# Optimization experiments

Measured on AMD Instinct MI355X. Metric: run time of the kernel, lower is better.

Reference implementation:

```python
import jax, jax.numpy as jnp
import numpy as np

T, B, D, H = 256, 128, 128, 1024
MEL = 48           # preprocess.melodyRange
MELODY_COEFF = 0.5
FORGET_BIAS = 1.0  # TF BasicLSTMCell default


def setup_inputs() -> dict:
    key = jax.random.key(0)
    ks = jax.random.split(key, 8)
    s = 0.05
    return {
        "inSeq": jax.random.normal(ks[0], (T, B, D), dtype=jnp.float32),
        "targetSeq": jax.random.randint(ks[1], (T, B, 2), 0, MEL).astype(jnp.int64),
        "W1": jax.random.normal(ks[2], (D + H, 4 * H), dtype=jnp.float32) * s,
        "b1": jnp.zeros((4 * H,), dtype=jnp.float32),
        "W2": jax.random.normal(ks[3], (2 * H, 4 * H), dtype=jnp.float32) * s,
        "b2": jnp.zeros((4 * H,), dtype=jnp.float32),
        "outW": jax.random.normal(ks[4], (H, D), dtype=jnp.float32) * s,
        "outB": jnp.zeros((D,), dtype=jnp.float32),
    }


def _lstm_cell(x, c, h, W, b):
    # TF BasicLSTMCell: gates in (i, j, f, o) order, forget_bias added to f
    z = jnp.concatenate([x, h], axis=-1) @ W + b
    i, j, f, o = jnp.split(z, 4, axis=-1)
    c_new = c * jax.nn.sigmoid(f + FORGET_BIAS) + jax.nn.sigmoid(i) * jnp.tanh(j)
    h_new = jnp.tanh(c_new) * jax.nn.sigmoid(o)
    return c_new, h_new


def _forward(inSeq, targetSeq, W1, b1, W2, b2, outW, outB):
    dt = inSeq.dtype
    zero = jnp.zeros((B, H), dtype=dt)

    def step(carry, x):
        c1, h1, c2, h2 = carry
        c1, h1 = _lstm_cell(x, c1, h1, W1, b1)
        c2, h2 = _lstm_cell(h1, c2, h2, W2, b2)
        return (c1, h1, c2, h2), h2

    _, outputs = jax.lax.scan(step, (zero, zero, zero, zero), inSeq)  # [T,B,H]
    logits = outputs @ outW + outB                                    # [T,B,D]

    mel_logits = logits[..., :MEL]
    har_logits = logits[..., MEL:]

    # probs: per-timestep dual softmax, concatenated
    probs = jnp.concatenate(
        [jax.nn.softmax(mel_logits, axis=-1), jax.nn.softmax(har_logits, axis=-1)],
        axis=-1,
    )

    # dual sparse softmax cross-entropy
    mel_lp = jax.nn.log_softmax(mel_logits, axis=-1)
    har_lp = jax.nn.log_softmax(har_logits, axis=-1)
    mel_ce = -jnp.take_along_axis(mel_lp, targetSeq[..., 0:1], axis=-1)[..., 0]
    har_ce = -jnp.take_along_axis(har_lp, targetSeq[..., 1:2], axis=-1)[..., 0]
    losses = MELODY_COEFF * mel_ce + (1.0 - MELODY_COEFF) * har_ce
    loss = jnp.sum(losses) / T / B
    return probs, loss


def reference(inSeq, targetSeq, W1, b1, W2, b2, outW, outB):
    return _forward(inSeq, targetSeq, W1, b1, W2, b2, outW, outB)
```

## Files before the change

kernel.cpp:

```cpp
#include <hip/hip_runtime.h>
#include <cstdint>
#include <cstddef>

#define T_ 256
#define B_ 128
#define D_ 128
#define H_ 1024
#define K1_ 1152
#define K2_ 2048

#define R_ 32

typedef __bf16 bf16x8 __attribute__((ext_vector_type(8)));
typedef short s8 __attribute__((ext_vector_type(8)));
typedef float f32x4 __attribute__((ext_vector_type(4)));

__device__ __forceinline__ unsigned short f2bf(float f) {
  unsigned int u = __builtin_bit_cast(unsigned int, f);
  u += 0x7fff + ((u >> 16) & 1);
  return (unsigned short)(u >> 16);
}
__device__ __forceinline__ float sigm(float x) { return 1.f / (1.f + __expf(-x)); }
__device__ __forceinline__ float tanh_(float x) { return 1.f - 2.f / (__expf(2.f * x) + 1.f); }

__device__ __forceinline__ f32x4 mfma16(s8 a, s8 b, f32x4 c) {
  return __builtin_amdgcn_mfma_f32_16x16x32_bf16(
      __builtin_bit_cast(bf16x8, a), __builtin_bit_cast(bf16x8, b), c, 0, 0, 0);
}

__device__ __forceinline__ void st_bypass_short(unsigned short* p, unsigned int v) {
  asm volatile("global_store_short %0, %1, off sc0 sc1" :: "v"(p), "v"(v) : "memory");
}
__device__ __forceinline__ void st_flag(int* p, int v) {
  asm volatile("global_store_dword %0, %1, off sc0 sc1" :: "v"(p), "v"(v) : "memory");
}

__device__ __forceinline__ void wave_wait1(const int* p, int want) {
  for (;;) {
    int4 v;
    asm volatile("global_load_dwordx4 %0, %1, off sc0 sc1\n\ts_waitcnt vmcnt(0)"
                 : "=v"(v) : "v"(p) : "memory");
    int ok = (v.x >= want) && (v.y >= want) && (v.z >= want) && (v.w >= want);
    if (__all(ok)) break;
    __builtin_amdgcn_s_sleep(1);
  }
}
__device__ __forceinline__ void wave_wait2(const int* pa, int wa,
                                           const int* pb, int wb) {
  for (;;) {
    int4 a, b;
    asm volatile("global_load_dwordx4 %0, %2, off sc0 sc1\n\t"
                 "global_load_dwordx4 %1, %3, off sc0 sc1\n\t"
                 "s_waitcnt vmcnt(0)"
                 : "=v"(a), "=v"(b) : "v"(pa), "v"(pb) : "memory");
    int ok = (a.x >= wa) && (a.y >= wa) && (a.z >= wa) && (a.w >= wa) &&
             (b.x >= wb) && (b.y >= wb) && (b.z >= wb) && (b.w >= wb);
    if (__all(ok)) break;
    __builtin_amdgcn_s_sleep(1);
  }
}

__global__ void prep_misc(const float* __restrict__ inSeq,
                          const float* __restrict__ outW,
                          unsigned short* __restrict__ xbf,
                          unsigned short* __restrict__ outWp,
                          unsigned short* __restrict__ h1b,
                          unsigned short* __restrict__ h1r,
                          unsigned short* __restrict__ h2all,
                          float* __restrict__ c1, float* __restrict__ c2,
                          float* __restrict__ loss,
                          int* __restrict__ f1, int* __restrict__ f2)
{
  int i = blockIdx.x * 256 + threadIdx.x;
  if (i < T_ * B_ * D_) xbf[i] = f2bf(inSeq[i]);
  if (i < B_ * H_) {
    c1[i] = 0.f; c2[i] = 0.f;
    h1b[B_ * H_ + i] = 0;
    if (h1r) h1r[(size_t)(R_ - 1) * B_ * H_ + i] = 0;
    h2all[i] = 0;
  }
  if (i < H_ * D_) {
    int c = i >> 10, k = i & 1023;
    outWp[i] = f2bf(outW[(size_t)k * D_ + c]);
  }
  if (f1 && i < 256) { f1[i] = 0; f2[i] = 0; }
  if (i == 0) loss[0] = 0.f;
}

__global__ void pack_w(const float* __restrict__ src, unsigned short* __restrict__ dst, int K)
{
  __shared__ float tile[64][65];
  int k0 = blockIdx.x * 64, j0 = blockIdx.y * 64, g = blockIdx.z;
  int tid = threadIdx.x;
#pragma unroll
  for (int e = 0; e < 16; ++e) {
    int li = e * 256 + tid;
    int kl = li >> 6, jl = li & 63;
    tile[kl][jl] = src[(size_t)(k0 + kl) * 4096 + g * 1024 + j0 + jl];
  }
  __syncthreads();
#pragma unroll
  for (int e = 0; e < 16; ++e) {
    int li = e * 256 + tid;
    int jl = li >> 6, kl = li & 63;
    dst[(size_t)((j0 + jl) * 4 + g) * K + k0 + kl] = f2bf(tile[kl][jl]);
  }
}

__global__ __launch_bounds__(256, 2) void phase_kernel(
    int p,
    const unsigned short* __restrict__ xbf,
    const unsigned short* __restrict__ W1p,
    const unsigned short* __restrict__ W2p,
    const float* __restrict__ b1,
    const float* __restrict__ b2,
    unsigned short* __restrict__ h1b,
    unsigned short* __restrict__ h2all,
    float* __restrict__ c1,
    float* __restrict__ c2)
{
  __shared__ float red[4][2048];
  const int bid = blockIdx.x;
  const bool isL2 = bid >= 256;
  if (!isL2 && p >= T_) return;
  if (isL2 && p == 0) return;
  const int jb = isL2 ? (bid - 256) : bid;
  const int mt = jb & 1, nt = jb >> 1;
  const int t = isL2 ? (p - 1) : p;
  const int r0 = mt * 64, c0 = nt * 32;
  const int tid = threadIdx.x;
  const int wid = tid >> 6, lane = tid & 63;
  const int quad = lane >> 4, l15 = lane & 15;
  const int kseg = quad * 8;

  const unsigned short* hsrc = h1b + (size_t)((p + 1) & 1) * (B_ * H_);

  f32x4 acc[4][2];
#pragma unroll
  for (int i = 0; i < 4; ++i)
#pragma unroll
    for (int j = 0; j < 2; ++j) acc[i][j] = (f32x4){0.f, 0.f, 0.f, 0.f};

  int arow[4], bcol[2];
#pragma unroll
  for (int i = 0; i < 4; ++i) arow[i] = r0 + i * 16 + l15;
#pragma unroll
  for (int j = 0; j < 2; ++j) bcol[j] = c0 + j * 16 + l15;

  if (!isL2) {
    const unsigned short* xt = xbf + (size_t)t * (B_ * D_);
    const int cpw = 9;
    const int kcbase = wid * cpw;
    s8 a[4], b[2], an[4], bn[2];
    auto LD = [&](int kc, s8* A, s8* Bv) {
      int kk = kc * 32 + kseg;
      if (kk < D_) {
#pragma unroll
        for (int i = 0; i < 4; ++i) A[i] = *(const s8*)(xt + (size_t)arow[i] * D_ + kk);
      } else {
#pragma unroll
        for (int i = 0; i < 4; ++i) A[i] = *(const s8*)(hsrc + (size_t)arow[i] * H_ + (kk - D_));
      }
#pragma unroll
      for (int j = 0; j < 2; ++j) Bv[j] = *(const s8*)(W1p + (size_t)bcol[j] * K1_ + kk);
    };
    LD(kcbase, a, b);
    for (int c = 0; c < cpw; ++c) {
      if (c + 1 < cpw) LD(kcbase + c + 1, an, bn);
#pragma unroll
      for (int i = 0; i < 4; ++i)
#pragma unroll
        for (int j = 0; j < 2; ++j) acc[i][j] = mfma16(a[i], b[j], acc[i][j]);
#pragma unroll
      for (int i = 0; i < 4; ++i) a[i] = an[i];
      b[0] = bn[0]; b[1] = bn[1];
    }
  } else {
    const unsigned short* h2prev = h2all + (size_t)t * (B_ * H_);
    const int cpw = 16;
    const int kcbase = wid * cpw;
    s8 a[4], b[2], an[4], bn[2];
    auto LD = [&](int kc, s8* A, s8* Bv) {
      int kk = kc * 32 + kseg;
      if (kk < H_) {
#pragma unroll
        for (int i = 0; i < 4; ++i) A[i] = *(const s8*)(hsrc + (size_t)arow[i] * H_ + kk);
      } else {
#pragma unroll
        for (int i = 0; i < 4; ++i) A[i] = *(const s8*)(h2prev + (size_t)arow[i] * H_ + (kk - H_));
      }
#pragma unroll
      for (int j = 0; j < 2; ++j) Bv[j] = *(const s8*)(W2p + (size_t)bcol[j] * K2_ + kk);
    };
    LD(kcbase, a, b);
    for (int c = 0; c < cpw; ++c) {
      if (c + 1 < cpw) LD(kcbase + c + 1, an, bn);
#pragma unroll
      for (int i = 0; i < 4; ++i)
#pragma unroll
        for (int j = 0; j < 2; ++j) acc[i][j] = mfma16(a[i], b[j], acc[i][j]);
#pragma unroll
      for (int i = 0; i < 4; ++i) a[i] = an[i];
      b[0] = bn[0]; b[1] = bn[1];
    }
  }

#pragma unroll
  for (int i = 0; i < 4; ++i)
#pragma unroll
    for (int j = 0; j < 2; ++j)
#pragma unroll
      for (int r = 0; r < 4; ++r)
        red[wid][(i * 16 + quad * 4 + r) * 32 + (j * 16 + l15)] = acc[i][j][r];
  __syncthreads();
#pragma unroll
  for (int it = 0; it < 8; ++it) {
    int e = it * 256 + tid;
    red[0][e] = red[0][e] + red[1][e] + red[2][e] + red[3][e];
  }
  __syncthreads();

  const float* bias = isL2 ? b2 : b1;
  float* cst = isL2 ? c2 : c1;
  unsigned short* hout = isL2 ? (h2all + (size_t)(t + 1) * (B_ * H_))
                              : (h1b + (size_t)(p & 1) * (B_ * H_));
#pragma unroll
  for (int it = 0; it < 2; ++it) {
    int s = it * 256 + tid;
    int row = s >> 3, u = s & 7;
    int jg = (c0 >> 2) + u;
    float zi = red[0][row * 32 + u * 4 + 0] + bias[0 * H_ + jg];
    float zj = red[0][row * 32 + u * 4 + 1] + bias[1 * H_ + jg];
    float zf = red[0][row * 32 + u * 4 + 2] + bias[2 * H_ + jg];
    float zo = red[0][row * 32 + u * 4 + 3] + bias[3 * H_ + jg];
    int rg = r0 + row;
    float co = cst[(size_t)rg * H_ + jg];
    float cn = co * sigm(zf + 1.0f) + sigm(zi) * tanh_(zj);
    float hn = tanh_(cn) * sigm(zo);
    cst[(size_t)rg * H_ + jg] = cn;
    hout[(size_t)rg * H_ + jg] = f2bf(hn);
  }
}

__global__ __launch_bounds__(256, 2) void lstm_persistent(
    const unsigned short* __restrict__ xbf,
    const unsigned short* __restrict__ W1p,
    const unsigned short* __restrict__ W2p,
    const float* __restrict__ b1,
    const float* __restrict__ b2,
    unsigned short* __restrict__ h1r,
    unsigned short* __restrict__ h2all,
    int* __restrict__ f1,
    int* __restrict__ f2)
{
  __shared__ float red[4][2048];
  const int bid = blockIdx.x;
  const bool isL2 = bid >= 256;
  const int jb = isL2 ? (bid - 256) : bid;
  const int mt = jb & 1, nt = jb >> 1;
  const int r0 = mt * 64, c0 = nt * 32;
  const int tid = threadIdx.x;
  const int wid = tid >> 6, lane = tid & 63;
  const int quad = lane >> 4, l15 = lane & 15;
  const int kseg = quad * 8;
  const int lane4 = lane * 4;

  int arow[4], bcol[2];
#pragma unroll
  for (int i = 0; i < 4; ++i) arow[i] = r0 + i * 16 + l15;
#pragma unroll
  for (int j = 0; j < 2; ++j) bcol[j] = c0 + j * 16 + l15;

  const float* bias = isL2 ? b2 : b1;
  int ridx[2];
  unsigned hoff[2];
  float bz[2][4], creg[2];
#pragma unroll
  for (int it = 0; it < 2; ++it) {
    int s = it * 256 + tid;
    int row = s >> 3, u = s & 7;
    int jg = (c0 >> 2) + u;
    ridx[it] = row * 32 + u * 4;
    hoff[it] = (unsigned)((r0 + row) * H_ + jg);
#pragma unroll
    for (int g = 0; g < 4; ++g) bz[it][g] = bias[g * H_ + jg];
    creg[it] = 0.f;
  }

  if (!isL2) {
    const int kcbase = wid * 9;
    s8 bw[9][2];
#pragma unroll
    for (int c = 0; c < 9; ++c) {
      int kk = (kcbase + c) * 32 + kseg;
      bw[c][0] = *(const s8*)(W1p + (size_t)bcol[0] * K1_ + kk);
      bw[c][1] = *(const s8*)(W1p + (size_t)bcol[1] * K1_ + kk);
    }
#pragma unroll
    for (int c = 0; c < 9; ++c)
      asm volatile("" : "+v"(bw[c][0]), "+v"(bw[c][1]));

    for (int t = 0; t < T_; ++t) {
      wave_wait2(f1 + lane4, t, f2 + lane4, t - (R_ - 1));
      if ((t & (R_ - 1)) == 0 && t)
        __builtin_amdgcn_fence(__ATOMIC_ACQUIRE, "agent");

      const unsigned short* hsrc = h1r + (size_t)((t + R_ - 1) & (R_ - 1)) * (B_ * H_);
      const unsigned short* xt = xbf + (size_t)t * (B_ * D_);
      f32x4 acc[4][2];
#pragma unroll
      for (int i = 0; i < 4; ++i)
#pragma unroll
        for (int j = 0; j < 2; ++j) acc[i][j] = (f32x4){0.f, 0.f, 0.f, 0.f};
      s8 a[4], an[4];
      auto LD = [&](int kc, s8* A) {
        int kk = kc * 32 + kseg;
        if (kk < D_) {
#pragma unroll
          for (int i = 0; i < 4; ++i) A[i] = *(const s8*)(xt + (size_t)arow[i] * D_ + kk);
        } else {
#pragma unroll
          for (int i = 0; i < 4; ++i) A[i] = *(const s8*)(hsrc + (size_t)arow[i] * H_ + (kk - D_));
        }
      };
      LD(kcbase, a);
#pragma unroll
      for (int c = 0; c < 9; ++c) {
        if (c + 1 < 9) LD(kcbase + c + 1, an);
#pragma unroll
        for (int i = 0; i < 4; ++i)
#pragma unroll
          for (int j = 0; j < 2; ++j) acc[i][j] = mfma16(a[i], bw[c][j], acc[i][j]);
#pragma unroll
        for (int i = 0; i < 4; ++i) a[i] = an[i];
      }
#pragma unroll
      for (int i = 0; i < 4; ++i)
#pragma unroll
        for (int j = 0; j < 2; ++j)
#pragma unroll
          for (int r = 0; r < 4; ++r)
            red[wid][(i * 16 + quad * 4 + r) * 32 + (j * 16 + l15)] = acc[i][j][r];
      __syncthreads();
#pragma unroll
      for (int it = 0; it < 8; ++it) {
        int e = it * 256 + tid;
        red[0][e] = red[0][e] + red[1][e] + red[2][e] + red[3][e];
      }
      __syncthreads();
      unsigned short* hout = h1r + (size_t)(t & (R_ - 1)) * (B_ * H_);
#pragma unroll
      for (int it = 0; it < 2; ++it) {
        float zi = red[0][ridx[it] + 0] + bz[it][0];
        float zj = red[0][ridx[it] + 1] + bz[it][1];
        float zf = red[0][ridx[it] + 2] + bz[it][2];
        float zo = red[0][ridx[it] + 3] + bz[it][3];
        float cn = creg[it] * sigm(zf + 1.0f) + sigm(zi) * tanh_(zj);
        float hn = tanh_(cn) * sigm(zo);
        creg[it] = cn;
        st_bypass_short(hout + hoff[it], (unsigned int)f2bf(hn));
      }
      asm volatile("s_waitcnt vmcnt(0)" ::: "memory");
      __syncthreads();
      if (tid == 0) st_flag(f1 + bid, t + 1);
    }
  } else {
    const int kcbase = wid * 16;
    s8 bw[16][2];
#pragma unroll
    for (int c = 0; c < 16; ++c) {
      int kk = (kcbase + c) * 32 + kseg;
      bw[c][0] = *(const s8*)(W2p + (size_t)bcol[0] * K2_ + kk);
      bw[c][1] = *(const s8*)(W2p + (size_t)bcol[1] * K2_ + kk);
    }
#pragma unroll
    for (int c = 0; c < 16; ++c)
      asm volatile("" : "+v"(bw[c][0]), "+v"(bw[c][1]));

    for (int t = 0; t < T_; ++t) {
      if (wid < 2) wave_wait1(f1 + lane4, t + 1);
      else         wave_wait1(f2 + lane4, t);
      if ((t & (R_ - 1)) == 0 && t)
        __builtin_amdgcn_fence(__ATOMIC_ACQUIRE, "agent");

      const unsigned short* hsrc = h1r + (size_t)(t & (R_ - 1)) * (B_ * H_);
      const unsigned short* h2prev = h2all + (size_t)t * (B_ * H_);
      f32x4 acc[4][2];
#pragma unroll
      for (int i = 0; i < 4; ++i)
#pragma unroll
        for (int j = 0; j < 2; ++j) acc[i][j] = (f32x4){0.f, 0.f, 0.f, 0.f};
      s8 a[4], an[4];
      auto LD = [&](int kc, s8* A) {
        int kk = kc * 32 + kseg;
        if (kk < H_) {
#pragma unroll
          for (int i = 0; i < 4; ++i) A[i] = *(const s8*)(hsrc + (size_t)arow[i] * H_ + kk);
        } else {
#pragma unroll
          for (int i = 0; i < 4; ++i) A[i] = *(const s8*)(h2prev + (size_t)arow[i] * H_ + (kk - H_));
        }
      };
      LD(kcbase, a);
#pragma unroll
      for (int c = 0; c < 16; ++c) {
        if (c + 1 < 16) LD(kcbase + c + 1, an);
#pragma unroll
        for (int i = 0; i < 4; ++i)
#pragma unroll
          for (int j = 0; j < 2; ++j) acc[i][j] = mfma16(a[i], bw[c][j], acc[i][j]);
#pragma unroll
        for (int i = 0; i < 4; ++i) a[i] = an[i];
      }
#pragma unroll
      for (int i = 0; i < 4; ++i)
#pragma unroll
        for (int j = 0; j < 2; ++j)
#pragma unroll
          for (int r = 0; r < 4; ++r)
            red[wid][(i * 16 + quad * 4 + r) * 32 + (j * 16 + l15)] = acc[i][j][r];
      __syncthreads();
#pragma unroll
      for (int it = 0; it < 8; ++it) {
        int e = it * 256 + tid;
        red[0][e] = red[0][e] + red[1][e] + red[2][e] + red[3][e];
      }
      __syncthreads();
      unsigned short* hout = h2all + (size_t)(t + 1) * (B_ * H_);
#pragma unroll
      for (int it = 0; it < 2; ++it) {
        float zi = red[0][ridx[it] + 0] + bz[it][0];
        float zj = red[0][ridx[it] + 1] + bz[it][1];
        float zf = red[0][ridx[it] + 2] + bz[it][2];
        float zo = red[0][ridx[it] + 3] + bz[it][3];
        float cn = creg[it] * sigm(zf + 1.0f) + sigm(zi) * tanh_(zj);
        float hn = tanh_(cn) * sigm(zo);
        creg[it] = cn;
        st_bypass_short(hout + hoff[it], (unsigned int)f2bf(hn));
      }
      asm volatile("s_waitcnt vmcnt(0)" ::: "memory");
      __syncthreads();
      if (tid == 0) st_flag(f2 + bid - 256, t + 1);
    }
  }
}

__global__ __launch_bounds__(256, 1) void proj_kernel(
    const unsigned short* __restrict__ h2flat,
    const unsigned short* __restrict__ outWp,
    const float* __restrict__ outB,
    const int* __restrict__ targets,
    float* __restrict__ out,
    float* __restrict__ loss)
{
  __shared__ float lg[128][129];
  __shared__ float red2[256];
  const int r0 = blockIdx.x * 128;
  const int tid = threadIdx.x;
  const int wid = tid >> 6, lane = tid & 63;
  const int quad = lane >> 4, l15 = lane & 15;
  const int wr = (wid & 1) * 64, wc = (wid >> 1) * 64;
  const int kseg = quad * 8;

  f32x4 acc[4][4];
#pragma unroll
  for (int i = 0; i < 4; ++i)
#pragma unroll
    for (int j = 0; j < 4; ++j) acc[i][j] = (f32x4){0.f, 0.f, 0.f, 0.f};

  int arow[4], bcolv[4];
#pragma unroll
  for (int i = 0; i < 4; ++i) arow[i] = r0 + wr + i * 16 + l15;
#pragma unroll
  for (int j = 0; j < 4; ++j) bcolv[j] = wc + j * 16 + l15;

  s8 a[4], b[4], an[4], bn[4];
  auto LD = [&](int kc, s8* A, s8* Bv) {
    int kk = kc * 32 + kseg;
#pragma unroll
    for (int i = 0; i < 4; ++i) A[i] = *(const s8*)(h2flat + (size_t)arow[i] * H_ + kk);
#pragma unroll
    for (int j = 0; j < 4; ++j) Bv[j] = *(const s8*)(outWp + (size_t)bcolv[j] * H_ + kk);
  };
  LD(0, a, b);
  for (int c = 0; c < 32; ++c) {
    if (c + 1 < 32) LD(c + 1, an, bn);
#pragma unroll
    for (int i = 0; i < 4; ++i)
#pragma unroll
      for (int j = 0; j < 4; ++j) acc[i][j] = mfma16(a[i], b[j], acc[i][j]);
#pragma unroll
    for (int i = 0; i < 4; ++i) a[i] = an[i];
#pragma unroll
    for (int j = 0; j < 4; ++j) b[j] = bn[j];
  }

#pragma unroll
  for (int i = 0; i < 4; ++i)
#pragma unroll
    for (int j = 0; j < 4; ++j)
#pragma unroll
      for (int r = 0; r < 4; ++r)
        lg[wr + i * 16 + quad * 4 + r][wc + j * 16 + l15] = acc[i][j][r] + outB[bcolv[j]];
  __syncthreads();

  const int row = tid >> 1, half = tid & 1;
  const int cbeg = half ? 48 : 0, cend = half ? 128 : 48;
  float m = -1e30f;
  for (int c = cbeg; c < cend; ++c) m = fmaxf(m, lg[row][c]);
  float s = 0.f;
  for (int c = cbeg; c < cend; ++c) s += __expf(lg[row][c] - m);
  float rinv = 1.f / s;
  float* orow = out + (size_t)(r0 + row) * D_;
  for (int c = cbeg; c < cend; ++c) orow[c] = __expf(lg[row][c] - m) * rinv;

  int tg = targets[(size_t)(r0 + row) * 2 + half];
  int tc = half ? (48 + tg) : tg;
  float ce = -(lg[row][tc] - m - logf(s));
  red2[tid] = 0.5f * ce;
  __syncthreads();
  for (int o = 128; o > 0; o >>= 1) {
    if (tid < o) red2[tid] += red2[tid + o];
    __syncthreads();
  }
  if (tid == 0) atomicAdd(loss, red2[0]);
}

__global__ void finalize_loss(const float* __restrict__ loss, float* __restrict__ out)
{
  out[(size_t)T_ * B_ * D_] = loss[0] * (1.f / (float)(T_ * B_));
}

extern "C" void kernel_launch(void* const* d_in, const int* in_sizes, int n_in,
                              void* d_out, int out_size, void* d_ws, size_t ws_size,
                              hipStream_t stream)
{
  const float* inSeq = (const float*)d_in[0];
  const int* targets = (const int*)d_in[1];
  const float* W1 = (const float*)d_in[2];
  const float* b1 = (const float*)d_in[3];
  const float* W2 = (const float*)d_in[4];
  const float* b2 = (const float*)d_in[5];
  const float* outW = (const float*)d_in[6];
  const float* outB = (const float*)d_in[7];
  float* out = (float*)d_out;

  char* w = (char*)d_ws;
  auto alloc = [&](size_t bytes) {
    char* r = w;
    w += (bytes + 255) & ~(size_t)255;
    return r;
  };
  unsigned short* W1p = (unsigned short*)alloc((size_t)4096 * K1_ * 2);
  unsigned short* W2p = (unsigned short*)alloc((size_t)4096 * K2_ * 2);
  unsigned short* xbf = (unsigned short*)alloc((size_t)T_ * B_ * D_ * 2);
  unsigned short* h1b = (unsigned short*)alloc((size_t)2 * B_ * H_ * 2);
  unsigned short* h2all = (unsigned short*)alloc((size_t)(T_ + 1) * B_ * H_ * 2);
  float* c1 = (float*)alloc((size_t)B_ * H_ * 4);
  float* c2 = (float*)alloc((size_t)B_ * H_ * 4);
  unsigned short* outWp = (unsigned short*)alloc((size_t)H_ * D_ * 2);
  float* loss = (float*)alloc(256);
  int* f1 = (int*)alloc(256 * 4);
  int* f2 = (int*)alloc(256 * 4);
  unsigned short* h1r = (unsigned short*)alloc((size_t)R_ * B_ * H_ * 2);

  const bool fits = ((size_t)(w - (char*)d_ws) <= ws_size);
  if (!fits) { f1 = nullptr; f2 = nullptr; h1r = nullptr; }

  prep_misc<<<dim3((T_ * B_ * D_) / 256), dim3(256), 0, stream>>>(
      inSeq, outW, xbf, outWp, h1b, h1r, h2all, c1, c2, loss, f1, f2);
  pack_w<<<dim3(K1_ / 64, 16, 4), dim3(256), 0, stream>>>(W1, W1p, K1_);
  pack_w<<<dim3(K2_ / 64, 16, 4), dim3(256), 0, stream>>>(W2, W2p, K2_);

  hipError_t ce = hipErrorUnknown;
  if (fits) {
    void* kargs[] = {(void*)&xbf, (void*)&W1p, (void*)&W2p, (void*)&b1,
                     (void*)&b2,  (void*)&h1r, (void*)&h2all,
                     (void*)&f1,  (void*)&f2};
    ce = hipLaunchCooperativeKernel((const void*)lstm_persistent,
                                    dim3(512), dim3(256), kargs, 0, stream);
  }
  if (ce != hipSuccess) {
    (void)hipGetLastError();
    for (int p = 0; p <= T_; ++p)
      phase_kernel<<<dim3(512), dim3(256), 0, stream>>>(
          p, xbf, W1p, W2p, b1, b2, h1b, h2all, c1, c2);
  }

  proj_kernel<<<dim3(256), dim3(256), 0, stream>>>(
      h2all + (size_t)B_ * H_, outWp, outB, targets, out, loss);
  finalize_loss<<<dim3(1), dim3(1), 0, stream>>>(loss, out);
}
```

Baseline: 5.515 ms.

## Wait only on flags of blocks producing needed K-slice and deepen A prefetch

Reworks the inter-block spin-wait so each wave polls just the flags of the blocks that wrote the K-range it reads. It uses a per-lane flag gather with one dword load per lane, replacing the blanket check over all blocks, and drops the s_sleep backoff. Flag slots are re-indexed by jb/mt, so the flag layout changes. The A-operand load pipeline goes from double to triple buffering to hide more global load latency. This risks more polling traffic without the sleep and depends on the new flag index mapping being consistent.

New measurement: 5.808 ms. +5.3%, slower.

```diff
diff --git a/kernel.cpp b/kernel.cpp
--- a/kernel.cpp
+++ b/kernel.cpp
@@ -14,6 +14,7 @@
 typedef __bf16 bf16x8 __attribute__((ext_vector_type(8)));
 typedef short s8 __attribute__((ext_vector_type(8)));
 typedef float f32x4 __attribute__((ext_vector_type(4)));
+typedef int i32x4 __attribute__((ext_vector_type(4)));
 
 __device__ __forceinline__ unsigned short f2bf(float f) {
   unsigned int u = __builtin_bit_cast(unsigned int, f);
@@ -33,31 +34,6 @@
 }
 __device__ __forceinline__ void st_flag(int* p, int v) {
   asm volatile("global_store_dword %0, %1, off sc0 sc1" :: "v"(p), "v"(v) : "memory");
-}
-
-__device__ __forceinline__ void wave_wait1(const int* p, int want) {
-  for (;;) {
-    int4 v;
-    asm volatile("global_load_dwordx4 %0, %1, off sc0 sc1\n\ts_waitcnt vmcnt(0)"
-                 : "=v"(v) : "v"(p) : "memory");
-    int ok = (v.x >= want) && (v.y >= want) && (v.z >= want) && (v.w >= want);
-    if (__all(ok)) break;
-    __builtin_amdgcn_s_sleep(1);
-  }
-}
-__device__ __forceinline__ void wave_wait2(const int* pa, int wa,
-                                           const int* pb, int wb) {
-  for (;;) {
-    int4 a, b;
-    asm volatile("global_load_dwordx4 %0, %2, off sc0 sc1\n\t"
-                 "global_load_dwordx4 %1, %3, off sc0 sc1\n\t"
-                 "s_waitcnt vmcnt(0)"
-                 : "=v"(a), "=v"(b) : "v"(pa), "v"(pb) : "memory");
-    int ok = (a.x >= wa) && (a.y >= wa) && (a.z >= wa) && (a.w >= wa) &&
-             (b.x >= wb) && (b.y >= wb) && (b.z >= wb) && (b.w >= wb);
-    if (__all(ok)) break;
-    __builtin_amdgcn_s_sleep(1);
-  }
 }
 
 __global__ void prep_misc(const float* __restrict__ inSeq,
@@ -300,8 +276,27 @@
     for (int c = 0; c < 9; ++c)
       asm volatile("" : "+v"(bw[c][0]), "+v"(bw[c][1]));
 
+    const int sbase = wid ? (20 + 36 * (wid - 1)) : 0;
+    const int sn = wid ? 36 : 20;
+    const int* sf = f1 + (2 * (sbase + (lane < sn ? lane : 0)) + mt);
+    const int* g1 = f1 + lane4;
+    const int* g2 = f2 + lane4;
+
     for (int t = 0; t < T_; ++t) {
-      wave_wait2(f1 + lane4, t, f2 + lane4, t - (R_ - 1));
+      const int wg = t - (R_ - 1);
+      for (;;) {
+        int v; i32x4 w1, w2;
+        asm volatile("global_load_dword %0, %3, off sc0 sc1\n\t"
+                     "global_load_dwordx4 %1, %4, off sc0 sc1\n\t"
+                     "global_load_dwordx4 %2, %5, off sc0 sc1\n\t"
+                     "s_waitcnt vmcnt(0)"
+                     : "=v"(v), "=v"(w1), "=v"(w2)
+                     : "v"(sf), "v"(g1), "v"(g2) : "memory");
+        int ok = ((lane >= sn) || (v >= t)) &&
+                 (w1.x >= wg) && (w1.y >= wg) && (w1.z >= wg) && (w1.w >= wg) &&
+                 (w2.x >= wg) && (w2.y >= wg) && (w2.z >= wg) && (w2.w >= wg);
+        if (__all(ok)) break;
+      }
       if ((t & (R_ - 1)) == 0 && t)
         __builtin_amdgcn_fence(__ATOMIC_ACQUIRE, "agent");
 
@@ -312,7 +307,7 @@
       for (int i = 0; i < 4; ++i)
 #pragma unroll
         for (int j = 0; j < 2; ++j) acc[i][j] = (f32x4){0.f, 0.f, 0.f, 0.f};
-      s8 a[4], an[4];
+      s8 ab[3][4];
       auto LD = [&](int kc, s8* A) {
         int kk = kc * 32 + kseg;
         if (kk < D_) {
@@ -323,16 +318,15 @@
           for (int i = 0; i < 4; ++i) A[i] = *(const s8*)(hsrc + (size_t)arow[i] * H_ + (kk - D_));
         }
       };
-      LD(kcbase, a);
+      LD(kcbase + 0, ab[0]);
+      LD(kcbase + 1, ab[1]);
 #pragma unroll
       for (int c = 0; c < 9; ++c) {
-        if (c + 1 < 9) LD(kcbase + c + 1, an);
+        if (c + 2 < 9) LD(kcbase + c + 2, ab[(c + 2) % 3]);
 #pragma unroll
         for (int i = 0; i < 4; ++i)
 #pragma unroll
-          for (int j = 0; j < 2; ++j) acc[i][j] = mfma16(a[i], bw[c][j], acc[i][j]);
-#pragma unroll
-        for (int i = 0; i < 4; ++i) a[i] = an[i];
+          for (int j = 0; j < 2; ++j) acc[i][j] = mfma16(ab[c % 3][i], bw[c][j], acc[i][j]);
       }
 #pragma unroll
       for (int i = 0; i < 4; ++i)
@@ -362,7 +356,7 @@
       }
       asm volatile("s_waitcnt vmcnt(0)" ::: "memory");
       __syncthreads();
-      if (tid == 0) st_flag(f1 + bid, t + 1);
+      if (tid == 0) st_flag(f1 + jb, t + 1);
     }
   } else {
     const int kcbase = wid * 16;
@@ -377,9 +371,19 @@
     for (int c = 0; c < 16; ++c)
       asm volatile("" : "+v"(bw[c][0]), "+v"(bw[c][1]));
 
+    const int* sf = (wid < 2)
+        ? (f1 + (2 * (64 * wid + lane) + mt))
+        : (f2 + (2 * (64 * (wid - 2) + lane) + mt));
+
     for (int t = 0; t < T_; ++t) {
-      if (wid < 2) wave_wait1(f1 + lane4, t + 1);
-      else         wave_wait1(f2 + lane4, t);
+      const int want = (wid < 2) ? (t + 1) : t;
+      for (;;) {
+        int v;
+        asm volatile("global_load_dword %0, %1, off sc0 sc1\n\t"
+                     "s_waitcnt vmcnt(0)"
+                     : "=v"(v) : "v"(sf) : "memory");
+        if (__all(v >= want)) break;
+      }
       if ((t & (R_ - 1)) == 0 && t)
         __builtin_amdgcn_fence(__ATOMIC_ACQUIRE, "agent");
 
@@ -390,7 +394,7 @@
       for (int i = 0; i < 4; ++i)
 #pragma unroll
         for (int j = 0; j < 2; ++j) acc[i][j] = (f32x4){0.f, 0.f, 0.f, 0.f};
-      s8 a[4], an[4];
+      s8 ab[3][4];
       auto LD = [&](int kc, s8* A) {
         int kk = kc * 32 + kseg;
         if (kk < H_) {
@@ -401,16 +405,15 @@
           for (int i = 0; i < 4; ++i) A[i] = *(const s8*)(h2prev + (size_t)arow[i] * H_ + (kk - H_));
         }
       };
-      LD(kcbase, a);
+      LD(kcbase + 0, ab[0]);
+      LD(kcbase + 1, ab[1]);
 #pragma unroll
       for (int c = 0; c < 16; ++c) {
-        if (c + 1 < 16) LD(kcbase + c + 1, an);
+        if (c + 2 < 16) LD(kcbase + c + 2, ab[(c + 2) % 3]);
 #pragma unroll
         for (int i = 0; i < 4; ++i)
 #pragma unroll
-          for (int j = 0; j < 2; ++j) acc[i][j] = mfma16(a[i], bw[c][j], acc[i][j]);
-#pragma unroll
-        for (int i = 0; i < 4; ++i) a[i] = an[i];
+          for (int j = 0; j < 2; ++j) acc[i][j] = mfma16(ab[c % 3][i], bw[c][j], acc[i][j]);
       }
 #pragma unroll
       for (int i = 0; i < 4; ++i)
@@ -440,7 +443,7 @@
       }
       asm volatile("s_waitcnt vmcnt(0)" ::: "memory");
       __syncthreads();
-      if (tid == 0) st_flag(f2 + bid - 256, t + 1);
+      if (tid == 0) st_flag(f2 + jb, t + 1);
     }
   }
 }
```
